# Performance work log

Measured on AMD Instinct MI355X. Metric: run time of the kernel, lower is better.

The kernel has to match this reference:

```python
import jax, jax.numpy as jnp
import numpy as np

KERNEL_SIZES = (3, 5, 7)
NUM_HEAD = 6
DIM = 192
K_SCALES = 3
HEADS_PER_SCALE = NUM_HEAD // K_SCALES  # 2
HEAD_DIM = DIM // NUM_HEAD              # 32
SCALE = HEAD_DIM ** -0.5


def _nbr_idx(L, K):
    # NATTEN non-causal, dilation=1: window centered on query, clamped at edges.
    start = jnp.clip(jnp.arange(L) - K // 2, 0, L - K)
    return start[:, None] + jnp.arange(K)  # [L, K]


def _na3d_branch(xi, K):
    # xi: [B, D, H, W, C] with C = 3 * HEADS_PER_SCALE * HEAD_DIM
    B, D, H, W, C = xi.shape
    qkv = xi.reshape(B, D, H, W, 3, HEADS_PER_SCALE, HEAD_DIM).transpose(4, 0, 5, 1, 2, 3, 6)
    q, k, v = qkv[0] * SCALE, qkv[1], qkv[2]  # each [B, h, D, H, W, hd]

    idd, idh, idw = _nbr_idx(D, K), _nbr_idx(H, K), _nbr_idx(W, K)

    def gather(t):
        t = jnp.take(t, idd, axis=2)  # [B,h,D,K,H,W,hd]
        t = jnp.take(t, idh, axis=4)  # [B,h,D,K,H,K,W,hd]
        t = jnp.take(t, idw, axis=6)  # [B,h,D,K,H,K,W,K,hd]
        return t

    kn = gather(k)
    vn = gather(v)
    # attention logits over the K^3 neighborhood per query
    attn = jnp.einsum('bndhwc,bndihjwkc->bndhwijk', q, kn)
    attn = jax.nn.softmax(attn.reshape(B, HEADS_PER_SCALE, D, H, W, K ** 3), axis=-1)
    attn = attn.reshape(B, HEADS_PER_SCALE, D, H, W, K, K, K)
    y = jnp.einsum('bndhwijk,bndihjwkc->bndhwc', attn, vn)
    # [B,h,D,H,W,hd] -> [B,D,H,W,h*hd]
    return y.transpose(0, 2, 3, 4, 1, 5).reshape(B, D, H, W, HEADS_PER_SCALE * HEAD_DIM)


def setup_inputs() -> dict:
    key = jax.random.key(0)
    k0, k1, k2 = jax.random.split(key, 3)
    x = jax.random.normal(k0, (1, 8, 24, 24, DIM), dtype=jnp.float32)
    W_qkv = jax.random.normal(k1, (DIM, 3 * DIM), dtype=jnp.float32) * 0.02
    b_qkv = jnp.zeros((3 * DIM,), dtype=jnp.float32)
    W_proj = jax.random.normal(k2, (DIM, DIM), dtype=jnp.float32) * 0.02
    b_proj = jnp.zeros((DIM,), dtype=jnp.float32)
    return {'x': x, 'W_qkv': W_qkv, 'b_qkv': b_qkv, 'W_proj': W_proj, 'b_proj': b_proj}


def reference(x, W_qkv, b_qkv, W_proj, b_proj):
    qkv = x @ W_qkv + b_qkv  # [B,D,H,W,3*DIM]
    # torch.split with channels [DIM, DIM, DIM]
    chunks = jnp.split(qkv, K_SCALES, axis=4)
    ys = [_na3d_branch(chunks[i], KERNEL_SIZES[i]) for i in range(K_SCALES)]
    y = jnp.concatenate(ys, axis=4)  # [B,D,H,W,DIM]
    return y @ W_proj + b_proj
```

## Files before the change

### kernel.cpp

```cpp
#include <hip/hip_runtime.h>

typedef unsigned short ushort_t;
typedef unsigned int uint_t;
typedef __attribute__((ext_vector_type(8))) short short8;
typedef __attribute__((ext_vector_type(4))) float f32x4;

constexpr int DD = 8, HH = 24, WW = 24;
constexpr int NQ = DD * HH * WW;
constexpr int CIN = 192;
constexpr int CQKV = 576;
constexpr int KP = 576;
constexpr float ATT_SCALE = 0.17677669529663687f;
constexpr int NROW = DD * HH;

__device__ __forceinline__ ushort_t bf16h(float x) {
    uint_t u = __float_as_uint(x);
    u += 0x7FFFu + ((u >> 16) & 1u);
    return (ushort_t)(u >> 16);
}
__device__ __forceinline__ float bf16f(ushort_t h) {
    return __uint_as_float(((uint_t)h) << 16);
}
__device__ __forceinline__ void unpack8(uint4 u, float* f) {
    f[0] = __uint_as_float(u.x << 16); f[1] = __uint_as_float(u.x & 0xffff0000u);
    f[2] = __uint_as_float(u.y << 16); f[3] = __uint_as_float(u.y & 0xffff0000u);
    f[4] = __uint_as_float(u.z << 16); f[5] = __uint_as_float(u.z & 0xffff0000u);
    f[6] = __uint_as_float(u.w << 16); f[7] = __uint_as_float(u.w & 0xffff0000u);
}

__global__ __launch_bounds__(256)
void convert_w_kernel(const float* __restrict__ Wq, const float* __restrict__ Wp,
                      ushort_t* __restrict__ Bq, ushort_t* __restrict__ Bp)
{
    __shared__ float T[32][36];
    int b = blockIdx.x;
    const float* W; ushort_t* Bb; int N;
    int kt, nt;
    if (b < 108) { W = Wq; Bb = Bq; N = CQKV; kt = b % 6; nt = b / 6; }
    else         { b -= 108; W = Wp; Bb = Bp; N = CIN; kt = b % 6; nt = b / 6; }
    const int k0 = kt * 32, n0 = nt * 32;
    const int tid = threadIdx.x;

    #pragma unroll
    for (int p = 0; p < 4; ++p) {
        int e = p * 256 + tid;
        int r = e >> 5, c = e & 31;
        T[c][r] = W[(long)(k0 + r) * N + n0 + c];
    }
    __syncthreads();
    const int n = tid >> 3;
    const int k4 = (tid & 7) * 4;
    float4 v = *(const float4*)(&T[n][k4]);
    ushort4 hv, lv;
    hv.x = bf16h(v.x); lv.x = bf16h(v.x - bf16f(hv.x));
    hv.y = bf16h(v.y); lv.y = bf16h(v.y - bf16f(hv.y));
    hv.z = bf16h(v.z); lv.z = bf16h(v.z - bf16f(hv.z));
    hv.w = bf16h(v.w); lv.w = bf16h(v.w - bf16f(hv.w));
    ushort_t* row = Bb + (long)(n0 + n) * KP + k0 + k4;
    *(ushort4*)(row)           = hv;
    *(ushort4*)(row + CIN)     = hv;
    *(ushort4*)(row + 2 * CIN) = lv;
}

template<bool BF16OUT>
__global__ __launch_bounds__(256)
void gemm_mfma_kernel(const float* __restrict__ A, const ushort_t* __restrict__ Bb,
                      const float* __restrict__ bias, void* __restrict__ Cout, int N)
{
    __shared__ ushort_t As[64][72];
    __shared__ ushort_t Bs[64][72];
    __shared__ float Ct[64][68];

    const int tid = threadIdx.x;
    const int bm = blockIdx.x * 64;
    const int bn = blockIdx.y * 64;

    const int wv = tid >> 6;
    const int lane = tid & 63;
    const int lm = lane & 15;
    const int quad = lane >> 4;
    const int wr = (wv >> 1) * 32;
    const int wc = (wv & 1) * 32;

    const int ar = tid >> 4;
    const int ac4 = (tid & 15) * 4;
    const int br0 = tid >> 3;
    const int bc0 = (tid & 7) * 8;

    f32x4 acc[2][2] = {};

    for (int kk = 0; kk < KP; kk += 64) {
        const int p3 = kk / 192;
        const int k0 = kk - p3 * 192;
        float4 av[4];
        #pragma unroll
        for (int p = 0; p < 4; ++p)
            av[p] = *(const float4*)(A + (long)(bm + ar + p * 16) * CIN + k0 + ac4);
        uint4 b0 = *(const uint4*)(Bb + (long)(bn + br0) * KP + kk + bc0);
        uint4 b1 = *(const uint4*)(Bb + (long)(bn + br0 + 32) * KP + kk + bc0);
        __syncthreads();
        #pragma unroll
        for (int p = 0; p < 4; ++p) {
            float4 v = av[p];
            ushort4 hv;
            hv.x = bf16h(v.x); hv.y = bf16h(v.y); hv.z = bf16h(v.z); hv.w = bf16h(v.w);
            if (p3 == 1) {
                hv.x = bf16h(v.x - bf16f(hv.x));
                hv.y = bf16h(v.y - bf16f(hv.y));
                hv.z = bf16h(v.z - bf16f(hv.z));
                hv.w = bf16h(v.w - bf16f(hv.w));
            }
            *(ushort4*)(&As[ar + p * 16][ac4]) = hv;
        }
        *(uint4*)(&Bs[br0][bc0]) = b0;
        *(uint4*)(&Bs[br0 + 32][bc0]) = b1;
        __syncthreads();

        #pragma unroll
        for (int ks = 0; ks < 64; ks += 32) {
            short8 af0 = *(const short8*)(&As[wr + lm][ks + quad * 8]);
            short8 af1 = *(const short8*)(&As[wr + 16 + lm][ks + quad * 8]);
            short8 bf0 = *(const short8*)(&Bs[wc + lm][ks + quad * 8]);
            short8 bf1 = *(const short8*)(&Bs[wc + 16 + lm][ks + quad * 8]);
            acc[0][0] = __builtin_amdgcn_mfma_f32_16x16x32_bf16(af0, bf0, acc[0][0], 0, 0, 0);
            acc[0][1] = __builtin_amdgcn_mfma_f32_16x16x32_bf16(af0, bf1, acc[0][1], 0, 0, 0);
            acc[1][0] = __builtin_amdgcn_mfma_f32_16x16x32_bf16(af1, bf0, acc[1][0], 0, 0, 0);
            acc[1][1] = __builtin_amdgcn_mfma_f32_16x16x32_bf16(af1, bf1, acc[1][1], 0, 0, 0);
        }
    }

    #pragma unroll
    for (int tc = 0; tc < 2; ++tc) {
        const float bv = bias[bn + wc + tc * 16 + lm];
        #pragma unroll
        for (int tr = 0; tr < 2; ++tr) {
            #pragma unroll
            for (int reg = 0; reg < 4; ++reg)
                Ct[wr + tr * 16 + quad * 4 + reg][wc + tc * 16 + lm] = acc[tr][tc][reg] + bv;
        }
    }
    __syncthreads();
    const int orow = tid >> 4;
    const int oc4 = (tid & 15) * 4;
    #pragma unroll
    for (int p = 0; p < 4; ++p) {
        const int r = orow + p * 16;
        float4 v = *(const float4*)(&Ct[r][oc4]);
        if (BF16OUT) {
            ushort4 hv;
            hv.x = bf16h(v.x); hv.y = bf16h(v.y); hv.z = bf16h(v.z); hv.w = bf16h(v.w);
            *(ushort4*)((ushort_t*)Cout + (long)(bm + r) * N + bn + oc4) = hv;
        } else {
            *(float4*)((float*)Cout + (long)(bm + r) * N + bn + oc4) = v;
        }
    }
}

constexpr int KROW = 72;
constexpr int RBUF = WW * KROW;

constexpr int EB0 = 0;
constexpr int EB1 = NROW * 2 * WW * 2;
constexpr int EB2 = EB1 + NROW * 3 * WW * 2;
constexpr int ETOT = EB2 + NROW * 4 * WW * 2;

template<int K>
__device__ __forceinline__
void split_chunk(const ushort_t* __restrict__ qkv,
                 float* __restrict__ accs, float* __restrict__ stats,
                 int r, int c, int nchunks, int scale, int ebase,
                 int w, int hd, int d8, int tid,
                 ushort_t* __restrict__ ksh, ushort_t* __restrict__ vsh)
{
    const int i0 = 2 * c;
    const int ni = (K - i0) < 2 ? (K - i0) : 2;
    const int NT = ni * K;

    const int dq = r / HH, hq = r % HH;
    int sd = dq - K / 2; sd = sd < 0 ? 0 : (sd > DD - K ? DD - K : sd);
    int sh = hq - K / 2; sh = sh < 0 ? 0 : (sh > HH - K ? HH - K : sh);
    int sw = w  - K / 2; sw = sw < 0 ? 0 : (sw > WW - K ? WW - K : sw);

    const int q = (dq * HH + hq) * WW + w;

    uint4 qu = *(const uint4*)(qkv + (long)q * CQKV + scale * 192 + hd * 32 + d8 * 8);
    float qf[8];
    unpack8(qu, qf);
    #pragma unroll
    for (int t = 0; t < 8; ++t) qf[t] *= ATT_SCALE;

    const int lw = tid >> 3;
    const int c8 = (tid & 7) * 8;

    auto load_kv = [&](int buf, int t) {
        int i = i0 + t / K;
        int j = t - (t / K) * K;
        const ushort_t* p = qkv + (long)(((sd + i) * HH + (sh + j)) * WW + lw) * CQKV
                          + scale * 192 + c8;
        uint4 kk = *(const uint4*)(p + 64);
        uint4 vv = *(const uint4*)(p + 128);
        *(uint4*)(ksh + buf * RBUF + lw * KROW + c8) = kk;
        *(uint4*)(vsh + buf * RBUF + lw * KROW + c8) = vv;
    };

    float m = -1e30f, sum = 0.f;
    float acc[8] = {};
    const int choff = hd * 32 + d8 * 8;

    load_kv(0, 0);
    if (NT > 1) load_kv(1, 1);

    for (int t = 0; t < NT; ++t) {
        __syncthreads();
        if (t + 2 < NT) load_kv((t + 2) % 3, t + 2);

        const ushort_t* kb = ksh + (t % 3) * RBUF + choff;
        float lg[K];
        #pragma unroll
        for (int n = 0; n < K; ++n) {
            uint4 ku = *(const uint4*)(kb + (sw + n) * KROW);
            float kf[8];
            unpack8(ku, kf);
            float p = qf[0] * kf[0] + qf[1] * kf[1] + qf[2] * kf[2] + qf[3] * kf[3]
                    + qf[4] * kf[4] + qf[5] * kf[5] + qf[6] * kf[6] + qf[7] * kf[7];
            p += __shfl_xor(p, 1);
            p += __shfl_xor(p, 2);
            lg[n] = p;
        }
        float mloc = lg[0];
        #pragma unroll
        for (int n = 1; n < K; ++n) mloc = fmaxf(mloc, lg[n]);
        float mnew = fmaxf(m, mloc);
        float alpha = __expf(m - mnew);
        m = mnew;
        sum *= alpha;
        #pragma unroll
        for (int d = 0; d < 8; ++d) acc[d] *= alpha;

        const ushort_t* vb = vsh + (t % 3) * RBUF + choff;
        #pragma unroll
        for (int n = 0; n < K; ++n) {
            float pr = __expf(lg[n] - mnew);
            sum += pr;
            uint4 vu = *(const uint4*)(vb + (sw + n) * KROW);
            float vf[8];
            unpack8(vu, vf);
            #pragma unroll
            for (int d = 0; d < 8; ++d) acc[d] += pr * vf[d];
        }
    }

    const int e = ebase + ((r * nchunks + c) * WW + w) * 2 + hd;
    if (d8 == 0) {
        stats[2 * e]     = m;
        stats[2 * e + 1] = sum;
    }
    float* ap = accs + (long)e * 32 + d8 * 8;
    *(float4*)(ap)     = make_float4(acc[0], acc[1], acc[2], acc[3]);
    *(float4*)(ap + 4) = make_float4(acc[4], acc[5], acc[6], acc[7]);
}

__global__ __launch_bounds__(192)
void na3d_split_kernel(const ushort_t* __restrict__ qkv,
                       float* __restrict__ accs, float* __restrict__ stats)
{
    __shared__ alignas(16) ushort_t ksh[3 * RBUF];
    __shared__ alignas(16) ushort_t vsh[3 * RBUF];

    const int tid = threadIdx.x;
    const int w  = tid >> 3;
    const int hd = (tid >> 2) & 1;
    const int d8 = tid & 3;

    const int bid = blockIdx.x;
    if (bid < NROW * 4) {
        int r = bid >> 2, c = bid & 3;
        split_chunk<7>(qkv, accs, stats, r, c, 4, 2, EB2, w, hd, d8, tid, ksh, vsh);
    } else if (bid < NROW * 4 + NROW * 3) {
        int t = bid - NROW * 4;
        int r = t / 3, c = t - (t / 3) * 3;
        split_chunk<5>(qkv, accs, stats, r, c, 3, 1, EB1, w, hd, d8, tid, ksh, vsh);
    } else {
        int t = bid - NROW * 7;
        int r = t >> 1, c = t & 1;
        split_chunk<3>(qkv, accs, stats, r, c, 2, 0, EB0, w, hd, d8, tid, ksh, vsh);
    }
}

__global__ __launch_bounds__(256)
void na3d_combine_kernel(const float* __restrict__ accs,
                         const float* __restrict__ stats,
                         float* __restrict__ y)
{
    const int n = blockIdx.x * 256 + threadIdx.x;
    constexpr int PER_SCALE = NROW * WW * 2 * 8;
    const int scale = n / PER_SCALE;
    const int rem = n - scale * PER_SCALE;
    const int d4 = rem & 7;
    const int hd = (rem >> 3) & 1;
    const int t  = rem >> 4;
    const int w  = t % WW;
    const int row = t / WW;

    const int CK = scale == 0 ? 2 : (scale == 1 ? 3 : 4);
    const int ebase = scale == 0 ? EB0 : (scale == 1 ? EB1 : EB2);

    float mv[4], sv[4];
    float M = -1e30f;
    for (int c = 0; c < CK; ++c) {
        int e = ebase + ((row * CK + c) * WW + w) * 2 + hd;
        mv[c] = stats[2 * e];
        sv[c] = stats[2 * e + 1];
        M = fmaxf(M, mv[c]);
    }
    float S = 0.f;
    float4 o = make_float4(0.f, 0.f, 0.f, 0.f);
    for (int c = 0; c < CK; ++c) {
        int e = ebase + ((row * CK + c) * WW + w) * 2 + hd;
        float wgt = __expf(mv[c] - M);
        S += sv[c] * wgt;
        float4 a = *(const float4*)(accs + (long)e * 32 + d4 * 4);
        o.x += wgt * a.x; o.y += wgt * a.y; o.z += wgt * a.z; o.w += wgt * a.w;
    }
    const float rs = 1.0f / S;
    o.x *= rs; o.y *= rs; o.z *= rs; o.w *= rs;

    const int q = row * WW + w;
    *(float4*)(y + (long)q * CIN + scale * 64 + hd * 32 + d4 * 4) = o;
}

extern "C" void kernel_launch(void* const* d_in, const int* in_sizes, int n_in,
                              void* d_out, int out_size, void* d_ws, size_t ws_size,
                              hipStream_t stream)
{
    const float* x      = (const float*)d_in[0];
    const float* W_qkv  = (const float*)d_in[1];
    const float* b_qkv  = (const float*)d_in[2];
    const float* W_proj = (const float*)d_in[3];
    const float* b_proj = (const float*)d_in[4];
    float* out = (float*)d_out;

    float* accs    = (float*)d_ws;
    float* stats   = accs + (long)ETOT * 32;
    float* y       = stats + 2 * ETOT;
    ushort_t* qkvb = (ushort_t*)(y + (long)NQ * CIN);
    ushort_t* Wbq  = qkvb + (long)NQ * CQKV;
    ushort_t* Wbp  = Wbq + (long)CQKV * KP;

    convert_w_kernel<<<dim3(144), 256, 0, stream>>>(W_qkv, W_proj, Wbq, Wbp);

    gemm_mfma_kernel<true><<<dim3(NQ / 64, CQKV / 64), 256, 0, stream>>>(x, Wbq, b_qkv, qkvb, CQKV);

    na3d_split_kernel<<<dim3(NROW * (4 + 3 + 2)), 192, 0, stream>>>(qkvb, accs, stats);
    na3d_combine_kernel<<<dim3(3 * NQ * 16 / 256), 256, 0, stream>>>(accs, stats, y);

    gemm_mfma_kernel<false><<<dim3(NQ / 64, CIN / 64), 256, 0, stream>>>(y, Wbp, b_proj, out, CIN);
}
```

Baseline: 122.7 us.

## Fuse all stages into one persistent cooperative kernel with grid syncs

Replaces the five separate launches (weight conversion, QKV GEMM, split attention, combine, projection GEMM) with a single cooperative persistent kernel of 512 blocks of 384 threads. The stages are separated by grid-wide barriers and share one shared-memory union. This is meant to remove per-launch overhead and the gaps between kernels. In exchange, blocks run with idle threads: the GEMM uses only 256 of the 384 threads and attention only 192, occupancy is limited by the union's size, and each grid.sync has its own cost. A multi-kernel fallback is kept in case the cooperative launch fails.

```diff
diff --git a/kernel.cpp b/kernel.cpp
--- a/kernel.cpp
+++ b/kernel.cpp
@@ -1,4 +1,7 @@
 #include <hip/hip_runtime.h>
+#include <hip/hip_cooperative_groups.h>
+
+namespace cg = cooperative_groups;
 
 typedef unsigned short ushort_t;
 typedef unsigned int uint_t;
@@ -13,6 +16,8 @@
 constexpr float ATT_SCALE = 0.17677669529663687f;
 constexpr int NROW = DD * HH;
 
+constexpr int NBLK = 512;
+
 __device__ __forceinline__ ushort_t bf16h(float x) {
     uint_t u = __float_as_uint(x);
     u += 0x7FFFu + ((u >> 16) & 1u);
@@ -28,53 +33,66 @@
     f[6] = __uint_as_float(u.w << 16); f[7] = __uint_as_float(u.w & 0xffff0000u);
 }
 
-__global__ __launch_bounds__(256)
-void convert_w_kernel(const float* __restrict__ Wq, const float* __restrict__ Wp,
-                      ushort_t* __restrict__ Bq, ushort_t* __restrict__ Bp)
-{
-    __shared__ float T[32][36];
-    int b = blockIdx.x;
-    const float* W; ushort_t* Bb; int N;
-    int kt, nt;
+constexpr int KROW = 72;
+constexpr int RBUF = WW * KROW;
+
+struct SmemGemm { ushort_t As[64][72]; ushort_t Bs[64][72]; };
+struct SmemSplit { ushort_t ksh[3 * RBUF]; ushort_t vsh[3 * RBUF]; };
+union Smem {
+    SmemGemm g;
+    float Ct[64][68];
+    SmemSplit s;
+    float T[32][36];
+};
+
+constexpr int EB0 = 0;
+constexpr int EB1 = NROW * 2 * WW * 2;
+constexpr int EB2 = EB1 + NROW * 3 * WW * 2;
+constexpr int ETOT = EB2 + NROW * 4 * WW * 2;
+
+__device__ __forceinline__
+void dev_convert_w(const float* __restrict__ Wq, const float* __restrict__ Wp,
+                   ushort_t* __restrict__ Bq, ushort_t* __restrict__ Bp,
+                   int b, int tid, Smem* u)
+{
+    const float* W; ushort_t* Bb; int N; int kt, nt;
     if (b < 108) { W = Wq; Bb = Bq; N = CQKV; kt = b % 6; nt = b / 6; }
     else         { b -= 108; W = Wp; Bb = Bp; N = CIN; kt = b % 6; nt = b / 6; }
     const int k0 = kt * 32, n0 = nt * 32;
-    const int tid = threadIdx.x;
-
-    #pragma unroll
-    for (int p = 0; p < 4; ++p) {
-        int e = p * 256 + tid;
-        int r = e >> 5, c = e & 31;
-        T[c][r] = W[(long)(k0 + r) * N + n0 + c];
-    }
-    __syncthreads();
-    const int n = tid >> 3;
-    const int k4 = (tid & 7) * 4;
-    float4 v = *(const float4*)(&T[n][k4]);
-    ushort4 hv, lv;
-    hv.x = bf16h(v.x); lv.x = bf16h(v.x - bf16f(hv.x));
-    hv.y = bf16h(v.y); lv.y = bf16h(v.y - bf16f(hv.y));
-    hv.z = bf16h(v.z); lv.z = bf16h(v.z - bf16f(hv.z));
-    hv.w = bf16h(v.w); lv.w = bf16h(v.w - bf16f(hv.w));
-    ushort_t* row = Bb + (long)(n0 + n) * KP + k0 + k4;
-    *(ushort4*)(row)           = hv;
-    *(ushort4*)(row + CIN)     = hv;
-    *(ushort4*)(row + 2 * CIN) = lv;
+
+    if (tid < 256) {
+        #pragma unroll
+        for (int p = 0; p < 4; ++p) {
+            int e = p * 256 + tid;
+            int r = e >> 5, c = e & 31;
+            u->T[c][r] = W[(long)(k0 + r) * N + n0 + c];
+        }
+    }
+    __syncthreads();
+    if (tid < 256) {
+        const int n = tid >> 3;
+        const int k4 = (tid & 7) * 4;
+        float4 v = *(const float4*)(&u->T[n][k4]);
+        ushort4 hv, lv;
+        hv.x = bf16h(v.x); lv.x = bf16h(v.x - bf16f(hv.x));
+        hv.y = bf16h(v.y); lv.y = bf16h(v.y - bf16f(hv.y));
+        hv.z = bf16h(v.z); lv.z = bf16h(v.z - bf16f(hv.z));
+        hv.w = bf16h(v.w); lv.w = bf16h(v.w - bf16f(hv.w));
+        ushort_t* row = Bb + (long)(n0 + n) * KP + k0 + k4;
+        *(ushort4*)(row)           = hv;
+        *(ushort4*)(row + CIN)     = hv;
+        *(ushort4*)(row + 2 * CIN) = lv;
+    }
+    __syncthreads();
 }
 
 template<bool BF16OUT>
-__global__ __launch_bounds__(256)
-void gemm_mfma_kernel(const float* __restrict__ A, const ushort_t* __restrict__ Bb,
-                      const float* __restrict__ bias, void* __restrict__ Cout, int N)
-{
-    __shared__ ushort_t As[64][72];
-    __shared__ ushort_t Bs[64][72];
-    __shared__ float Ct[64][68];
-
-    const int tid = threadIdx.x;
-    const int bm = blockIdx.x * 64;
-    const int bn = blockIdx.y * 64;
-
+__device__ __forceinline__
+void dev_gemm_tile(const float* __restrict__ A, const ushort_t* __restrict__ Bb,
+                   const float* __restrict__ bias, void* __restrict__ Cout,
+                   int N, int tm, int tn, int tid, Smem* u)
+{
+    const int bm = tm * 64, bn = tn * 64;
     const int wv = tid >> 6;
     const int lane = tid & 63;
     const int lm = lane & 15;
@@ -92,86 +110,94 @@
     for (int kk = 0; kk < KP; kk += 64) {
         const int p3 = kk / 192;
         const int k0 = kk - p3 * 192;
-        float4 av[4];
+        float4 av[4]; uint4 b0, b1;
+        if (tid < 256) {
+            #pragma unroll
+            for (int p = 0; p < 4; ++p)
+                av[p] = *(const float4*)(A + (long)(bm + ar + p * 16) * CIN + k0 + ac4);
+            b0 = *(const uint4*)(Bb + (long)(bn + br0) * KP + kk + bc0);
+            b1 = *(const uint4*)(Bb + (long)(bn + br0 + 32) * KP + kk + bc0);
+        }
+        __syncthreads();
+        if (tid < 256) {
+            #pragma unroll
+            for (int p = 0; p < 4; ++p) {
+                float4 v = av[p];
+                ushort4 hv;
+                hv.x = bf16h(v.x); hv.y = bf16h(v.y); hv.z = bf16h(v.z); hv.w = bf16h(v.w);
+                if (p3 == 1) {
+                    hv.x = bf16h(v.x - bf16f(hv.x));
+                    hv.y = bf16h(v.y - bf16f(hv.y));
+                    hv.z = bf16h(v.z - bf16f(hv.z));
+                    hv.w = bf16h(v.w - bf16f(hv.w));
+                }
+                *(ushort4*)(&u->g.As[ar + p * 16][ac4]) = hv;
+            }
+            *(uint4*)(&u->g.Bs[br0][bc0]) = b0;
+            *(uint4*)(&u->g.Bs[br0 + 32][bc0]) = b1;
+        }
+        __syncthreads();
+
+        if (wv < 4) {
+            #pragma unroll
+            for (int ks = 0; ks < 64; ks += 32) {
+                short8 af0 = *(const short8*)(&u->g.As[wr + lm][ks + quad * 8]);
+                short8 af1 = *(const short8*)(&u->g.As[wr + 16 + lm][ks + quad * 8]);
+                short8 bf0 = *(const short8*)(&u->g.Bs[wc + lm][ks + quad * 8]);
+                short8 bf1 = *(const short8*)(&u->g.Bs[wc + 16 + lm][ks + quad * 8]);
+                acc[0][0] = __builtin_amdgcn_mfma_f32_16x16x32_bf16(af0, bf0, acc[0][0], 0, 0, 0);
+                acc[0][1] = __builtin_amdgcn_mfma_f32_16x16x32_bf16(af0, bf1, acc[0][1], 0, 0, 0);
+                acc[1][0] = __builtin_amdgcn_mfma_f32_16x16x32_bf16(af1, bf0, acc[1][0], 0, 0, 0);
+                acc[1][1] = __builtin_amdgcn_mfma_f32_16x16x32_bf16(af1, bf1, acc[1][1], 0, 0, 0);
+            }
+        }
+    }
+
+    __syncthreads();
+    if (wv < 4) {
         #pragma unroll
-        for (int p = 0; p < 4; ++p)
-            av[p] = *(const float4*)(A + (long)(bm + ar + p * 16) * CIN + k0 + ac4);
-        uint4 b0 = *(const uint4*)(Bb + (long)(bn + br0) * KP + kk + bc0);
-        uint4 b1 = *(const uint4*)(Bb + (long)(bn + br0 + 32) * KP + kk + bc0);
-        __syncthreads();
+        for (int tc = 0; tc < 2; ++tc) {
+            const float bv = bias[bn + wc + tc * 16 + lm];
+            #pragma unroll
+            for (int tr = 0; tr < 2; ++tr) {
+                #pragma unroll
+                for (int reg = 0; reg < 4; ++reg)
+                    u->Ct[wr + tr * 16 + quad * 4 + reg][wc + tc * 16 + lm] = acc[tr][tc][reg] + bv;
+            }
+        }
+    }
+    __syncthreads();
+    if (tid < 256) {
+        const int orow = tid >> 4;
+        const int oc4 = (tid & 15) * 4;
         #pragma unroll
         for (int p = 0; p < 4; ++p) {
-            float4 v = av[p];
-            ushort4 hv;
-            hv.x = bf16h(v.x); hv.y = bf16h(v.y); hv.z = bf16h(v.z); hv.w = bf16h(v.w);
-            if (p3 == 1) {
-                hv.x = bf16h(v.x - bf16f(hv.x));
-                hv.y = bf16h(v.y - bf16f(hv.y));
-                hv.z = bf16h(v.z - bf16f(hv.z));
-                hv.w = bf16h(v.w - bf16f(hv.w));
-            }
-            *(ushort4*)(&As[ar + p * 16][ac4]) = hv;
-        }
-        *(uint4*)(&Bs[br0][bc0]) = b0;
-        *(uint4*)(&Bs[br0 + 32][bc0]) = b1;
-        __syncthreads();
-
-        #pragma unroll
-        for (int ks = 0; ks < 64; ks += 32) {
-            short8 af0 = *(const short8*)(&As[wr + lm][ks + quad * 8]);
-            short8 af1 = *(const short8*)(&As[wr + 16 + lm][ks + quad * 8]);
-            short8 bf0 = *(const short8*)(&Bs[wc + lm][ks + quad * 8]);
-            short8 bf1 = *(const short8*)(&Bs[wc + 16 + lm][ks + quad * 8]);
-            acc[0][0] = __builtin_amdgcn_mfma_f32_16x16x32_bf16(af0, bf0, acc[0][0], 0, 0, 0);
-            acc[0][1] = __builtin_amdgcn_mfma_f32_16x16x32_bf16(af0, bf1, acc[0][1], 0, 0, 0);
-            acc[1][0] = __builtin_amdgcn_mfma_f32_16x16x32_bf16(af1, bf0, acc[1][0], 0, 0, 0);
-            acc[1][1] = __builtin_amdgcn_mfma_f32_16x16x32_bf16(af1, bf1, acc[1][1], 0, 0, 0);
-        }
-    }
-
-    #pragma unroll
-    for (int tc = 0; tc < 2; ++tc) {
-        const float bv = bias[bn + wc + tc * 16 + lm];
-        #pragma unroll
-        for (int tr = 0; tr < 2; ++tr) {
-            #pragma unroll
-            for (int reg = 0; reg < 4; ++reg)
-                Ct[wr + tr * 16 + quad * 4 + reg][wc + tc * 16 + lm] = acc[tr][tc][reg] + bv;
-        }
-    }
-    __syncthreads();
-    const int orow = tid >> 4;
-    const int oc4 = (tid & 15) * 4;
-    #pragma unroll
-    for (int p = 0; p < 4; ++p) {
-        const int r = orow + p * 16;
-        float4 v = *(const float4*)(&Ct[r][oc4]);
-        if (BF16OUT) {
-            ushort4 hv;
-            hv.x = bf16h(v.x); hv.y = bf16h(v.y); hv.z = bf16h(v.z); hv.w = bf16h(v.w);
-            *(ushort4*)((ushort_t*)Cout + (long)(bm + r) * N + bn + oc4) = hv;
-        } else {
-            *(float4*)((float*)Cout + (long)(bm + r) * N + bn + oc4) = v;
-        }
-    }
-}
-
-constexpr int KROW = 72;
-constexpr int RBUF = WW * KROW;
-
-constexpr int EB0 = 0;
-constexpr int EB1 = NROW * 2 * WW * 2;
-constexpr int EB2 = EB1 + NROW * 3 * WW * 2;
-constexpr int ETOT = EB2 + NROW * 4 * WW * 2;
+            const int r = orow + p * 16;
+            float4 v = *(const float4*)(&u->Ct[r][oc4]);
+            if (BF16OUT) {
+                ushort4 hv;
+                hv.x = bf16h(v.x); hv.y = bf16h(v.y); hv.z = bf16h(v.z); hv.w = bf16h(v.w);
+                *(ushort4*)((ushort_t*)Cout + (long)(bm + r) * N + bn + oc4) = hv;
+            } else {
+                *(float4*)((float*)Cout + (long)(bm + r) * N + bn + oc4) = v;
+            }
+        }
+    }
+    __syncthreads();
+}
 
 template<int K>
 __device__ __forceinline__
-void split_chunk(const ushort_t* __restrict__ qkv,
-                 float* __restrict__ accs, float* __restrict__ stats,
-                 int r, int c, int nchunks, int scale, int ebase,
-                 int w, int hd, int d8, int tid,
-                 ushort_t* __restrict__ ksh, ushort_t* __restrict__ vsh)
-{
+void dev_split_chunk(const ushort_t* __restrict__ qkv,
+                     float* __restrict__ accs, float* __restrict__ stats,
+                     int r, int c, int nchunks, int scale, int ebase,
+                     int tid, SmemSplit* s)
+{
+    const bool act = tid < 192;
+    const int w  = tid >> 3;
+    const int hd = (tid >> 2) & 1;
+    const int d8 = tid & 3;
+
     const int i0 = 2 * c;
     const int ni = (K - i0) < 2 ? (K - i0) : 2;
     const int NT = ni * K;
@@ -181,13 +207,14 @@
     int sh = hq - K / 2; sh = sh < 0 ? 0 : (sh > HH - K ? HH - K : sh);
     int sw = w  - K / 2; sw = sw < 0 ? 0 : (sw > WW - K ? WW - K : sw);
 
-    const int q = (dq * HH + hq) * WW + w;
-
-    uint4 qu = *(const uint4*)(qkv + (long)q * CQKV + scale * 192 + hd * 32 + d8 * 8);
     float qf[8];
-    unpack8(qu, qf);
-    #pragma unroll
-    for (int t = 0; t < 8; ++t) qf[t] *= ATT_SCALE;
+    if (act) {
+        const int q = (dq * HH + hq) * WW + w;
+        uint4 qu = *(const uint4*)(qkv + (long)q * CQKV + scale * 192 + hd * 32 + d8 * 8);
+        unpack8(qu, qf);
+        #pragma unroll
+        for (int t = 0; t < 8; ++t) qf[t] *= ATT_SCALE;
+    }
 
     const int lw = tid >> 3;
     const int c8 = (tid & 7) * 8;
@@ -199,100 +226,96 @@
                           + scale * 192 + c8;
         uint4 kk = *(const uint4*)(p + 64);
         uint4 vv = *(const uint4*)(p + 128);
-        *(uint4*)(ksh + buf * RBUF + lw * KROW + c8) = kk;
-        *(uint4*)(vsh + buf * RBUF + lw * KROW + c8) = vv;
+        *(uint4*)(s->ksh + buf * RBUF + lw * KROW + c8) = kk;
+        *(uint4*)(s->vsh + buf * RBUF + lw * KROW + c8) = vv;
     };
 
     float m = -1e30f, sum = 0.f;
     float acc[8] = {};
     const int choff = hd * 32 + d8 * 8;
 
-    load_kv(0, 0);
-    if (NT > 1) load_kv(1, 1);
+    if (act) {
+        load_kv(0, 0);
+        if (NT > 1) load_kv(1, 1);
+    }
 
     for (int t = 0; t < NT; ++t) {
         __syncthreads();
-        if (t + 2 < NT) load_kv((t + 2) % 3, t + 2);
-
-        const ushort_t* kb = ksh + (t % 3) * RBUF + choff;
-        float lg[K];
-        #pragma unroll
-        for (int n = 0; n < K; ++n) {
-            uint4 ku = *(const uint4*)(kb + (sw + n) * KROW);
-            float kf[8];
-            unpack8(ku, kf);
-            float p = qf[0] * kf[0] + qf[1] * kf[1] + qf[2] * kf[2] + qf[3] * kf[3]
-                    + qf[4] * kf[4] + qf[5] * kf[5] + qf[6] * kf[6] + qf[7] * kf[7];
-            p += __shfl_xor(p, 1);
-            p += __shfl_xor(p, 2);
-            lg[n] = p;
-        }
-        float mloc = lg[0];
-        #pragma unroll
-        for (int n = 1; n < K; ++n) mloc = fmaxf(mloc, lg[n]);
-        float mnew = fmaxf(m, mloc);
-        float alpha = __expf(m - mnew);
-        m = mnew;
-        sum *= alpha;
-        #pragma unroll
-        for (int d = 0; d < 8; ++d) acc[d] *= alpha;
-
-        const ushort_t* vb = vsh + (t % 3) * RBUF + choff;
-        #pragma unroll
-        for (int n = 0; n < K; ++n) {
-            float pr = __expf(lg[n] - mnew);
-            sum += pr;
-            uint4 vu = *(const uint4*)(vb + (sw + n) * KROW);
-            float vf[8];
-            unpack8(vu, vf);
-            #pragma unroll
-            for (int d = 0; d < 8; ++d) acc[d] += pr * vf[d];
-        }
-    }
-
-    const int e = ebase + ((r * nchunks + c) * WW + w) * 2 + hd;
-    if (d8 == 0) {
-        stats[2 * e]     = m;
-        stats[2 * e + 1] = sum;
-    }
-    float* ap = accs + (long)e * 32 + d8 * 8;
-    *(float4*)(ap)     = make_float4(acc[0], acc[1], acc[2], acc[3]);
-    *(float4*)(ap + 4) = make_float4(acc[4], acc[5], acc[6], acc[7]);
-}
-
-__global__ __launch_bounds__(192)
-void na3d_split_kernel(const ushort_t* __restrict__ qkv,
-                       float* __restrict__ accs, float* __restrict__ stats)
-{
-    __shared__ alignas(16) ushort_t ksh[3 * RBUF];
-    __shared__ alignas(16) ushort_t vsh[3 * RBUF];
-
-    const int tid = threadIdx.x;
-    const int w  = tid >> 3;
-    const int hd = (tid >> 2) & 1;
-    const int d8 = tid & 3;
-
-    const int bid = blockIdx.x;
-    if (bid < NROW * 4) {
-        int r = bid >> 2, c = bid & 3;
-        split_chunk<7>(qkv, accs, stats, r, c, 4, 2, EB2, w, hd, d8, tid, ksh, vsh);
-    } else if (bid < NROW * 4 + NROW * 3) {
-        int t = bid - NROW * 4;
+        if (act) {
+            if (t + 2 < NT) load_kv((t + 2) % 3, t + 2);
+
+            const ushort_t* kb = s->ksh + (t % 3) * RBUF + choff;
+            float lg[K];
+            #pragma unroll
+            for (int n = 0; n < K; ++n) {
+                uint4 ku = *(const uint4*)(kb + (sw + n) * KROW);
+                float kf[8];
+                unpack8(ku, kf);
+                float p = qf[0] * kf[0] + qf[1] * kf[1] + qf[2] * kf[2] + qf[3] * kf[3]
+                        + qf[4] * kf[4] + qf[5] * kf[5] + qf[6] * kf[6] + qf[7] * kf[7];
+                p += __shfl_xor(p, 1);
+                p += __shfl_xor(p, 2);
+                lg[n] = p;
+            }
+            float mloc = lg[0];
+            #pragma unroll
+            for (int n = 1; n < K; ++n) mloc = fmaxf(mloc, lg[n]);
+            float mnew = fmaxf(m, mloc);
+            float alpha = __expf(m - mnew);
+            m = mnew;
+            sum *= alpha;
+            #pragma unroll
+            for (int d = 0; d < 8; ++d) acc[d] *= alpha;
+
+            const ushort_t* vb = s->vsh + (t % 3) * RBUF + choff;
+            #pragma unroll
+            for (int n = 0; n < K; ++n) {
+                float pr = __expf(lg[n] - mnew);
+                sum += pr;
+                uint4 vu = *(const uint4*)(vb + (sw + n) * KROW);
+                float vf[8];
+                unpack8(vu, vf);
+                #pragma unroll
+                for (int d = 0; d < 8; ++d) acc[d] += pr * vf[d];
+            }
+        }
+    }
+    __syncthreads();
+
+    if (act) {
+        const int e = ebase + ((r * nchunks + c) * WW + w) * 2 + hd;
+        if (d8 == 0) {
+            stats[2 * e]     = m;
+            stats[2 * e + 1] = sum;
+        }
+        float* ap = accs + (long)e * 32 + d8 * 8;
+        *(float4*)(ap)     = make_float4(acc[0], acc[1], acc[2], acc[3]);
+        *(float4*)(ap + 4) = make_float4(acc[4], acc[5], acc[6], acc[7]);
+    }
+}
+
+__device__ __forceinline__
+void split_task(int task, const ushort_t* qkv, float* accs, float* stats,
+                int tid, SmemSplit* s)
+{
+    if (task < NROW * 4) {
+        int r = task >> 2, c = task & 3;
+        dev_split_chunk<7>(qkv, accs, stats, r, c, 4, 2, EB2, tid, s);
+    } else if (task < NROW * 7) {
+        int t = task - NROW * 4;
         int r = t / 3, c = t - (t / 3) * 3;
-        split_chunk<5>(qkv, accs, stats, r, c, 3, 1, EB1, w, hd, d8, tid, ksh, vsh);
+        dev_split_chunk<5>(qkv, accs, stats, r, c, 3, 1, EB1, tid, s);
     } else {
-        int t = bid - NROW * 7;
+        int t = task - NROW * 7;
         int r = t >> 1, c = t & 1;
-        split_chunk<3>(qkv, accs, stats, r, c, 2, 0, EB0, w, hd, d8, tid, ksh, vsh);
-    }
-}
-
-__global__ __launch_bounds__(256)
-void na3d_combine_kernel(const float* __restrict__ accs,
-                         const float* __restrict__ stats,
-                         float* __restrict__ y)
-{
-    const int n = blockIdx.x * 256 + threadIdx.x;
+        dev_split_chunk<3>(qkv, accs, stats, r, c, 2, 0, EB0, tid, s);
+    }
+}
+
+__device__ __forceinline__
+void dev_combine(const float* __restrict__ accs, const float* __restrict__ stats,
+                 float* __restrict__ y, int n)
+{
     constexpr int PER_SCALE = NROW * WW * 2 * 8;
     const int scale = n / PER_SCALE;
     const int rem = n - scale * PER_SCALE;
@@ -329,6 +352,68 @@
     *(float4*)(y + (long)q * CIN + scale * 64 + hd * 32 + d4 * 4) = o;
 }
 
+__global__ __launch_bounds__(384, 3)
+void mega_kernel(const float* x, const float* Wq, const float* bq,
+                 const float* Wp, const float* bp, float* out,
+                 float* accs, float* stats, float* y,
+                 ushort_t* qkvb, ushort_t* Bbq, ushort_t* Bbp)
+{
+    __shared__ Smem u;
+    cg::grid_group grid = cg::this_grid();
+    const int bid = blockIdx.x;
+    const int tid = threadIdx.x;
+
+    if (bid < 144) dev_convert_w(Wq, Wp, Bbq, Bbp, bid, tid, &u);
+    grid.sync();
+
+    for (int task = bid; task < 648; task += NBLK) {
+        dev_gemm_tile<true>(x, Bbq, bq, qkvb, CQKV, task % 72, task / 72, tid, &u);
+    }
+    grid.sync();
+
+    for (int task = bid; task < 1728; task += NBLK) {
+        split_task(task, qkvb, accs, stats, tid, &u.s);
+    }
+    grid.sync();
+
+    for (int task = bid; task < 576; task += NBLK) {
+        dev_combine(accs, stats, y, task * 384 + tid);
+    }
+    grid.sync();
+
+    if (bid < 216) {
+        dev_gemm_tile<false>(y, Bbp, bp, out, CIN, bid % 72, bid / 72, tid, &u);
+    }
+}
+
+__global__ __launch_bounds__(384, 3)
+void k_convert_w(const float* Wq, const float* Wp, ushort_t* Bq, ushort_t* Bp)
+{
+    __shared__ Smem u;
+    dev_convert_w(Wq, Wp, Bq, Bp, blockIdx.x, threadIdx.x, &u);
+}
+
+template<bool BF16OUT>
+__global__ __launch_bounds__(384, 3)
+void k_gemm(const float* A, const ushort_t* Bb, const float* bias, void* C, int N)
+{
+    __shared__ Smem u;
+    dev_gemm_tile<BF16OUT>(A, Bb, bias, C, N, blockIdx.x, blockIdx.y, threadIdx.x, &u);
+}
+
+__global__ __launch_bounds__(384, 3)
+void k_split(const ushort_t* qkv, float* accs, float* stats)
+{
+    __shared__ Smem u;
+    split_task(blockIdx.x, qkv, accs, stats, threadIdx.x, &u.s);
+}
+
+__global__ __launch_bounds__(384, 3)
+void k_combine(const float* accs, const float* stats, float* y)
+{
+    dev_combine(accs, stats, y, blockIdx.x * 384 + threadIdx.x);
+}
+
 extern "C" void kernel_launch(void* const* d_in, const int* in_sizes, int n_in,
                               void* d_out, int out_size, void* d_ws, size_t ws_size,
                               hipStream_t stream)
@@ -347,12 +432,17 @@
     ushort_t* Wbq  = qkvb + (long)NQ * CQKV;
     ushort_t* Wbp  = Wbq + (long)CQKV * KP;
 
-    convert_w_kernel<<<dim3(144), 256, 0, stream>>>(W_qkv, W_proj, Wbq, Wbp);
-
-    gemm_mfma_kernel<true><<<dim3(NQ / 64, CQKV / 64), 256, 0, stream>>>(x, Wbq, b_qkv, qkvb, CQKV);
-
-    na3d_split_kernel<<<dim3(NROW * (4 + 3 + 2)), 192, 0, stream>>>(qkvb, accs, stats);
-    na3d_combine_kernel<<<dim3(3 * NQ * 16 / 256), 256, 0, stream>>>(accs, stats, y);
-
-    gemm_mfma_kernel<false><<<dim3(NQ / 64, CIN / 64), 256, 0, stream>>>(y, Wbp, b_proj, out, CIN);
-}
+    void* args[] = {(void*)&x, (void*)&W_qkv, (void*)&b_qkv, (void*)&W_proj,
+                    (void*)&b_proj, (void*)&out, (void*)&accs, (void*)&stats,
+                    (void*)&y, (void*)&qkvb, (void*)&Wbq, (void*)&Wbp};
+    hipError_t err = hipLaunchCooperativeKernel((void*)mega_kernel,
+                                                dim3(NBLK), dim3(384),
+                                                args, 0, stream);
+    if (err != hipSuccess) {
+        k_convert_w<<<dim3(144), 384, 0, stream>>>(W_qkv, W_proj, Wbq, Wbp);
+        k_gemm<true><<<dim3(72, 9), 384, 0, stream>>>(x, Wbq, b_qkv, qkvb, CQKV);
+        k_split<<<dim3(1728), 384, 0, stream>>>(qkvb, accs, stats);
+        k_combine<<<dim3(576), 384, 0, stream>>>(accs, stats, y);
+        k_gemm<false><<<dim3(72, 3), 384, 0, stream>>>(y, Wbp, b_proj, out, CIN);
+    }
+}
```

Result: slower. 394.9 us (+221.9%).

## Fuse weight conversion into GEMMs and fuse softmax-combine into projection GEMM

Applied to the files above, without the earlier changes.

Drops the separate weight-conversion kernel: both GEMMs now read fp32 weights directly and split them into bf16 hi/lo on the fly while staging into shared memory, with a transposed scalar store. The combine step, which merges partial softmax chunks, is folded into the output projection GEMM, so the merged activations go to a 64x192 shared tile instead of a global y buffer. This cuts two launches and one global round trip. In exchange the combine work is repeated for each of the three N-tiles, and the transposed 2-byte shared stores may cause bank conflicts.

```diff
diff --git a/kernel.cpp b/kernel.cpp
--- a/kernel.cpp
+++ b/kernel.cpp
@@ -27,45 +27,28 @@
     f[4] = __uint_as_float(u.z << 16); f[5] = __uint_as_float(u.z & 0xffff0000u);
     f[6] = __uint_as_float(u.w << 16); f[7] = __uint_as_float(u.w & 0xffff0000u);
 }
+__device__ __forceinline__ short8 afrag8(const float* p, bool lo_phase) {
+    float4 a = *(const float4*)(p);
+    float4 b = *(const float4*)(p + 4);
+    float f[8] = {a.x, a.y, a.z, a.w, b.x, b.y, b.z, b.w};
+    short8 r;
+    #pragma unroll
+    for (int i = 0; i < 8; ++i) {
+        ushort_t h = bf16h(f[i]);
+        if (lo_phase) h = bf16h(f[i] - bf16f(h));
+        r[i] = (short)h;
+    }
+    return r;
+}
+
+constexpr int EB0 = 0;
+constexpr int EB1 = NROW * 2 * WW * 2;
+constexpr int EB2 = EB1 + NROW * 3 * WW * 2;
+constexpr int ETOT = EB2 + NROW * 4 * WW * 2;
 
 __global__ __launch_bounds__(256)
-void convert_w_kernel(const float* __restrict__ Wq, const float* __restrict__ Wp,
-                      ushort_t* __restrict__ Bq, ushort_t* __restrict__ Bp)
-{
-    __shared__ float T[32][36];
-    int b = blockIdx.x;
-    const float* W; ushort_t* Bb; int N;
-    int kt, nt;
-    if (b < 108) { W = Wq; Bb = Bq; N = CQKV; kt = b % 6; nt = b / 6; }
-    else         { b -= 108; W = Wp; Bb = Bp; N = CIN; kt = b % 6; nt = b / 6; }
-    const int k0 = kt * 32, n0 = nt * 32;
-    const int tid = threadIdx.x;
-
-    #pragma unroll
-    for (int p = 0; p < 4; ++p) {
-        int e = p * 256 + tid;
-        int r = e >> 5, c = e & 31;
-        T[c][r] = W[(long)(k0 + r) * N + n0 + c];
-    }
-    __syncthreads();
-    const int n = tid >> 3;
-    const int k4 = (tid & 7) * 4;
-    float4 v = *(const float4*)(&T[n][k4]);
-    ushort4 hv, lv;
-    hv.x = bf16h(v.x); lv.x = bf16h(v.x - bf16f(hv.x));
-    hv.y = bf16h(v.y); lv.y = bf16h(v.y - bf16f(hv.y));
-    hv.z = bf16h(v.z); lv.z = bf16h(v.z - bf16f(hv.z));
-    hv.w = bf16h(v.w); lv.w = bf16h(v.w - bf16f(hv.w));
-    ushort_t* row = Bb + (long)(n0 + n) * KP + k0 + k4;
-    *(ushort4*)(row)           = hv;
-    *(ushort4*)(row + CIN)     = hv;
-    *(ushort4*)(row + 2 * CIN) = lv;
-}
-
-template<bool BF16OUT>
-__global__ __launch_bounds__(256)
-void gemm_mfma_kernel(const float* __restrict__ A, const ushort_t* __restrict__ Bb,
-                      const float* __restrict__ bias, void* __restrict__ Cout, int N)
+void gemm1_kernel(const float* __restrict__ A, const float* __restrict__ W,
+                  const float* __restrict__ bias, ushort_t* __restrict__ Cout)
 {
     __shared__ ushort_t As[64][72];
     __shared__ ushort_t Bs[64][72];
@@ -74,6 +57,7 @@
     const int tid = threadIdx.x;
     const int bm = blockIdx.x * 64;
     const int bn = blockIdx.y * 64;
+    const int N = CQKV;
 
     const int wv = tid >> 6;
     const int lane = tid & 63;
@@ -84,20 +68,20 @@
 
     const int ar = tid >> 4;
     const int ac4 = (tid & 15) * 4;
-    const int br0 = tid >> 3;
-    const int bc0 = (tid & 7) * 8;
+    const int kr = ar;
+    const int nc4 = ac4;
 
     f32x4 acc[2][2] = {};
 
     for (int kk = 0; kk < KP; kk += 64) {
         const int p3 = kk / 192;
         const int k0 = kk - p3 * 192;
-        float4 av[4];
-        #pragma unroll
-        for (int p = 0; p < 4; ++p)
-            av[p] = *(const float4*)(A + (long)(bm + ar + p * 16) * CIN + k0 + ac4);
-        uint4 b0 = *(const uint4*)(Bb + (long)(bn + br0) * KP + kk + bc0);
-        uint4 b1 = *(const uint4*)(Bb + (long)(bn + br0 + 32) * KP + kk + bc0);
+        float4 av[4], wv4[4];
+        #pragma unroll
+        for (int p = 0; p < 4; ++p) {
+            av[p]  = *(const float4*)(A + (long)(bm + ar + p * 16) * CIN + k0 + ac4);
+            wv4[p] = *(const float4*)(W + (long)(k0 + kr + p * 16) * N + bn + nc4);
+        }
         __syncthreads();
         #pragma unroll
         for (int p = 0; p < 4; ++p) {
@@ -111,9 +95,21 @@
                 hv.w = bf16h(v.w - bf16f(hv.w));
             }
             *(ushort4*)(&As[ar + p * 16][ac4]) = hv;
-        }
-        *(uint4*)(&Bs[br0][bc0]) = b0;
-        *(uint4*)(&Bs[br0 + 32][bc0]) = b1;
+            float4 u = wv4[p];
+            ushort4 bw;
+            bw.x = bf16h(u.x); bw.y = bf16h(u.y); bw.z = bf16h(u.z); bw.w = bf16h(u.w);
+            if (p3 == 2) {
+                bw.x = bf16h(u.x - bf16f(bw.x));
+                bw.y = bf16h(u.y - bf16f(bw.y));
+                bw.z = bf16h(u.z - bf16f(bw.z));
+                bw.w = bf16h(u.w - bf16f(bw.w));
+            }
+            const int kc = kr + p * 16;
+            Bs[nc4 + 0][kc] = bw.x;
+            Bs[nc4 + 1][kc] = bw.y;
+            Bs[nc4 + 2][kc] = bw.z;
+            Bs[nc4 + 3][kc] = bw.w;
+        }
         __syncthreads();
 
         #pragma unroll
@@ -146,23 +142,14 @@
     for (int p = 0; p < 4; ++p) {
         const int r = orow + p * 16;
         float4 v = *(const float4*)(&Ct[r][oc4]);
-        if (BF16OUT) {
-            ushort4 hv;
-            hv.x = bf16h(v.x); hv.y = bf16h(v.y); hv.z = bf16h(v.z); hv.w = bf16h(v.w);
-            *(ushort4*)((ushort_t*)Cout + (long)(bm + r) * N + bn + oc4) = hv;
-        } else {
-            *(float4*)((float*)Cout + (long)(bm + r) * N + bn + oc4) = v;
-        }
+        ushort4 hv;
+        hv.x = bf16h(v.x); hv.y = bf16h(v.y); hv.z = bf16h(v.z); hv.w = bf16h(v.w);
+        *(ushort4*)(Cout + (long)(bm + r) * N + bn + oc4) = hv;
     }
 }
 
 constexpr int KROW = 72;
 constexpr int RBUF = WW * KROW;
-
-constexpr int EB0 = 0;
-constexpr int EB1 = NROW * 2 * WW * 2;
-constexpr int EB2 = EB1 + NROW * 3 * WW * 2;
-constexpr int ETOT = EB2 + NROW * 4 * WW * 2;
 
 template<int K>
 __device__ __forceinline__
@@ -288,45 +275,132 @@
 }
 
 __global__ __launch_bounds__(256)
-void na3d_combine_kernel(const float* __restrict__ accs,
-                         const float* __restrict__ stats,
-                         float* __restrict__ y)
+void combine_gemm2_kernel(const float* __restrict__ accs, const float* __restrict__ stats,
+                          const float* __restrict__ W, const float* __restrict__ bias,
+                          float* __restrict__ out)
 {
-    const int n = blockIdx.x * 256 + threadIdx.x;
-    constexpr int PER_SCALE = NROW * WW * 2 * 8;
-    const int scale = n / PER_SCALE;
-    const int rem = n - scale * PER_SCALE;
-    const int d4 = rem & 7;
-    const int hd = (rem >> 3) & 1;
-    const int t  = rem >> 4;
-    const int w  = t % WW;
-    const int row = t / WW;
-
-    const int CK = scale == 0 ? 2 : (scale == 1 ? 3 : 4);
-    const int ebase = scale == 0 ? EB0 : (scale == 1 ? EB1 : EB2);
-
-    float mv[4], sv[4];
-    float M = -1e30f;
-    for (int c = 0; c < CK; ++c) {
-        int e = ebase + ((row * CK + c) * WW + w) * 2 + hd;
-        mv[c] = stats[2 * e];
-        sv[c] = stats[2 * e + 1];
-        M = fmaxf(M, mv[c]);
-    }
-    float S = 0.f;
-    float4 o = make_float4(0.f, 0.f, 0.f, 0.f);
-    for (int c = 0; c < CK; ++c) {
-        int e = ebase + ((row * CK + c) * WW + w) * 2 + hd;
-        float wgt = __expf(mv[c] - M);
-        S += sv[c] * wgt;
-        float4 a = *(const float4*)(accs + (long)e * 32 + d4 * 4);
-        o.x += wgt * a.x; o.y += wgt * a.y; o.z += wgt * a.z; o.w += wgt * a.w;
-    }
-    const float rs = 1.0f / S;
-    o.x *= rs; o.y *= rs; o.z *= rs; o.w *= rs;
-
-    const int q = row * WW + w;
-    *(float4*)(y + (long)q * CIN + scale * 64 + hd * 32 + d4 * 4) = o;
+    __shared__ float ytile[64][196];
+    __shared__ ushort_t Bs[64][72];
+
+    const int tid = threadIdx.x;
+    const int bm = blockIdx.x * 64;
+    const int bn = blockIdx.y * 64;
+
+    {
+        const int ql = tid >> 2;
+        const int q = bm + ql;
+        const int row = q / WW;
+        const int w = q - row * WW;
+        const int chb = (tid & 3) * 48;
+        #pragma unroll
+        for (int c4 = 0; c4 < 12; ++c4) {
+            const int ch = chb + c4 * 4;
+            const int scale = ch >> 6;
+            const int rem = ch & 63;
+            const int hd = rem >> 5;
+            const int d4 = (rem >> 2) & 7;
+            const int CK = scale == 0 ? 2 : (scale == 1 ? 3 : 4);
+            const int ebase = scale == 0 ? EB0 : (scale == 1 ? EB1 : EB2);
+
+            float mv[4], sv[4];
+            float M = -1e30f;
+            for (int c = 0; c < CK; ++c) {
+                int e = ebase + ((row * CK + c) * WW + w) * 2 + hd;
+                mv[c] = stats[2 * e];
+                sv[c] = stats[2 * e + 1];
+                M = fmaxf(M, mv[c]);
+            }
+            float S = 0.f;
+            float4 o = make_float4(0.f, 0.f, 0.f, 0.f);
+            for (int c = 0; c < CK; ++c) {
+                int e = ebase + ((row * CK + c) * WW + w) * 2 + hd;
+                float wgt = __expf(mv[c] - M);
+                S += sv[c] * wgt;
+                float4 a = *(const float4*)(accs + (long)e * 32 + d4 * 4);
+                o.x += wgt * a.x; o.y += wgt * a.y; o.z += wgt * a.z; o.w += wgt * a.w;
+            }
+            const float rs = 1.0f / S;
+            o.x *= rs; o.y *= rs; o.z *= rs; o.w *= rs;
+            *(float4*)(&ytile[ql][ch]) = o;
+        }
+    }
+    __syncthreads();
+
+    const int wv = tid >> 6;
+    const int lane = tid & 63;
+    const int lm = lane & 15;
+    const int quad = lane >> 4;
+    const int wr = (wv >> 1) * 32;
+    const int wc = (wv & 1) * 32;
+
+    const int kr = tid >> 4;
+    const int nc4 = (tid & 15) * 4;
+
+    f32x4 acc[2][2] = {};
+
+    for (int kk = 0; kk < KP; kk += 64) {
+        const int p3 = kk / 192;
+        const int k0 = kk - p3 * 192;
+        float4 wv4[4];
+        #pragma unroll
+        for (int p = 0; p < 4; ++p)
+            wv4[p] = *(const float4*)(W + (long)(k0 + kr + p * 16) * CIN + bn + nc4);
+        __syncthreads();
+        #pragma unroll
+        for (int p = 0; p < 4; ++p) {
+            float4 u = wv4[p];
+            ushort4 bw;
+            bw.x = bf16h(u.x); bw.y = bf16h(u.y); bw.z = bf16h(u.z); bw.w = bf16h(u.w);
+            if (p3 == 2) {
+                bw.x = bf16h(u.x - bf16f(bw.x));
+                bw.y = bf16h(u.y - bf16f(bw.y));
+                bw.z = bf16h(u.z - bf16f(bw.z));
+                bw.w = bf16h(u.w - bf16f(bw.w));
+            }
+            const int kc = kr + p * 16;
+            Bs[nc4 + 0][kc] = bw.x;
+            Bs[nc4 + 1][kc] = bw.y;
+            Bs[nc4 + 2][kc] = bw.z;
+            Bs[nc4 + 3][kc] = bw.w;
+        }
+        __syncthreads();
+
+        const bool alo = (p3 == 1);
+        #pragma unroll
+        for (int ks = 0; ks < 64; ks += 32) {
+            short8 af0 = afrag8(&ytile[wr + lm][k0 + ks + quad * 8], alo);
+            short8 af1 = afrag8(&ytile[wr + 16 + lm][k0 + ks + quad * 8], alo);
+            short8 bf0 = *(const short8*)(&Bs[wc + lm][ks + quad * 8]);
+            short8 bf1 = *(const short8*)(&Bs[wc + 16 + lm][ks + quad * 8]);
+            acc[0][0] = __builtin_amdgcn_mfma_f32_16x16x32_bf16(af0, bf0, acc[0][0], 0, 0, 0);
+            acc[0][1] = __builtin_amdgcn_mfma_f32_16x16x32_bf16(af0, bf1, acc[0][1], 0, 0, 0);
+            acc[1][0] = __builtin_amdgcn_mfma_f32_16x16x32_bf16(af1, bf0, acc[1][0], 0, 0, 0);
+            acc[1][1] = __builtin_amdgcn_mfma_f32_16x16x32_bf16(af1, bf1, acc[1][1], 0, 0, 0);
+        }
+    }
+
+    __syncthreads();
+    float* Ct = &ytile[0][0];
+
+    #pragma unroll
+    for (int tc = 0; tc < 2; ++tc) {
+        const float bv = bias[bn + wc + tc * 16 + lm];
+        #pragma unroll
+        for (int tr = 0; tr < 2; ++tr) {
+            #pragma unroll
+            for (int reg = 0; reg < 4; ++reg)
+                Ct[(wr + tr * 16 + quad * 4 + reg) * 68 + wc + tc * 16 + lm] = acc[tr][tc][reg] + bv;
+        }
+    }
+    __syncthreads();
+    const int orow = tid >> 4;
+    const int oc4 = (tid & 15) * 4;
+    #pragma unroll
+    for (int p = 0; p < 4; ++p) {
+        const int r = orow + p * 16;
+        float4 v = *(const float4*)(&Ct[r * 68 + oc4]);
+        *(float4*)(out + (long)(bm + r) * CIN + bn + oc4) = v;
+    }
 }
 
 extern "C" void kernel_launch(void* const* d_in, const int* in_sizes, int n_in,
@@ -342,17 +416,11 @@
 
     float* accs    = (float*)d_ws;
     float* stats   = accs + (long)ETOT * 32;
-    float* y       = stats + 2 * ETOT;
-    ushort_t* qkvb = (ushort_t*)(y + (long)NQ * CIN);
-    ushort_t* Wbq  = qkvb + (long)NQ * CQKV;
-    ushort_t* Wbp  = Wbq + (long)CQKV * KP;
-
-    convert_w_kernel<<<dim3(144), 256, 0, stream>>>(W_qkv, W_proj, Wbq, Wbp);
-
-    gemm_mfma_kernel<true><<<dim3(NQ / 64, CQKV / 64), 256, 0, stream>>>(x, Wbq, b_qkv, qkvb, CQKV);
+    ushort_t* qkvb = (ushort_t*)(stats + 2 * ETOT);
+
+    gemm1_kernel<<<dim3(NQ / 64, CQKV / 64), 256, 0, stream>>>(x, W_qkv, b_qkv, qkvb);
 
     na3d_split_kernel<<<dim3(NROW * (4 + 3 + 2)), 192, 0, stream>>>(qkvb, accs, stats);
-    na3d_combine_kernel<<<dim3(3 * NQ * 16 / 256), 256, 0, stream>>>(accs, stats, y);
-
-    gemm_mfma_kernel<false><<<dim3(NQ / 64, CIN / 64), 256, 0, stream>>>(y, Wbp, b_proj, out, CIN);
-}
+
+    combine_gemm2_kernel<<<dim3(NQ / 64, CIN / 64), 256, 0, stream>>>(accs, stats, W_proj, b_proj, out);
+}
```

Measured after the change: 148.0 us. +20.6%, slower.
